# Kernel tuning notes

Hardware: AMD Instinct MI355X
Metric: run time of the kernel (lower is better)

The kernel has to match this reference:

```python
import jax, jax.numpy as jnp
import numpy as np

N_NODES = 20000
N_EDGES = 320000
NUM_FEATURES = 128
HIDDEN = 128
NUM_CLASSES = 40
GRID_SIZE = 4
SPLINE_ORDER = 3
NB = GRID_SIZE + SPLINE_ORDER  # basis functions per input feature
_H = 2.0 / GRID_SIZE  # grid_range [-1, 1]
GRID = jnp.arange(-SPLINE_ORDER, GRID_SIZE + SPLINE_ORDER + 1, dtype=jnp.float32) * _H - 1.0


def b_splines(x):
    # x: (N, in) -> (N, in, NB) via Cox-de Boor recursion (efficient-KAN)
    xg = x[..., None]
    b = ((xg >= GRID[:-1]) & (xg < GRID[1:])).astype(x.dtype)
    for k in range(1, SPLINE_ORDER + 1):
        b = ((xg - GRID[: -(k + 1)]) / (GRID[k:-1] - GRID[: -(k + 1)]) * b[..., :-1]
             + (GRID[k + 1:] - xg) / (GRID[k + 1:] - GRID[1:-k]) * b[..., 1:])
    return b


def kan_linear(x, base_w, spline_w):
    # base branch: silu(x) @ W_base^T ; spline branch: contraction over (in, NB)
    base = jax.nn.silu(x) @ base_w.T
    spline = jnp.einsum('nik,oik->no', b_splines(x), spline_w)
    return base + spline


def gcn_conv(h, base_w, spline_w, bias, src_f, dst_f, norm):
    h = kan_linear(h, base_w, spline_w)
    msg = h[src_f] * norm[:, None]  # gather + edge scaling
    out = jax.ops.segment_sum(msg, dst_f, num_segments=N_NODES)
    return out + bias


def batchnorm(h, gamma, beta):
    mean = h.mean(axis=0)
    var = h.var(axis=0)  # biased, as torch BN uses for normalization
    return (h - mean) * jax.lax.rsqrt(var + 1e-5) * gamma + beta


def setup_inputs() -> dict:
    key = jax.random.key(0)
    ks = jax.random.split(key, 8)
    s = 0.1
    return {
        'x': jax.random.normal(ks[0], (N_NODES, NUM_FEATURES), dtype=jnp.float32),
        'edge_index': jax.random.randint(ks[1], (2, N_EDGES), 0, N_NODES, dtype=jnp.int64),
        'base_w0': jax.random.normal(ks[2], (HIDDEN, NUM_FEATURES), dtype=jnp.float32) * s,
        'spline_w0': jax.random.normal(ks[3], (HIDDEN, NUM_FEATURES, NB), dtype=jnp.float32) * s,
        'bias0': jnp.zeros((HIDDEN,), dtype=jnp.float32),
        'base_w1': jax.random.normal(ks[4], (HIDDEN, HIDDEN), dtype=jnp.float32) * s,
        'spline_w1': jax.random.normal(ks[5], (HIDDEN, HIDDEN, NB), dtype=jnp.float32) * s,
        'bias1': jnp.zeros((HIDDEN,), dtype=jnp.float32),
        'base_w_out': jax.random.normal(ks[6], (NUM_CLASSES, NUM_FEATURES + 2 * HIDDEN), dtype=jnp.float32) * s,
        'spline_w_out': jax.random.normal(ks[7], (NUM_CLASSES, NUM_FEATURES + 2 * HIDDEN, NB), dtype=jnp.float32) * s,
        'bias_out': jnp.zeros((NUM_CLASSES,), dtype=jnp.float32),
        'gamma': jnp.ones((HIDDEN,), dtype=jnp.float32),
        'beta': jnp.zeros((HIDDEN,), dtype=jnp.float32),
    }


def reference(x, edge_index, base_w0, spline_w0, bias0, base_w1, spline_w1, bias1,
              base_w_out, spline_w_out, bias_out, gamma, beta):
    # gcn_norm with self loops (computed once, reused by every layer)
    loop = jnp.arange(N_NODES, dtype=edge_index.dtype)
    src_f = jnp.concatenate([edge_index[0], loop])
    dst_f = jnp.concatenate([edge_index[1], loop])
    deg = jax.ops.segment_sum(jnp.ones_like(dst_f, dtype=x.dtype), dst_f, num_segments=N_NODES)
    dinv = jnp.where(deg > 0, jax.lax.rsqrt(jnp.maximum(deg, 1e-12)), 0.0)
    norm = dinv[src_f] * dinv[dst_f]

    skips = [x]
    h = x
    for bw, sw, b in ((base_w0, spline_w0, bias0), (base_w1, spline_w1, bias1)):
        h = gcn_conv(h, bw, sw, b, src_f, dst_f, norm)
        h = batchnorm(h, gamma, beta)  # shared BN, dropout p=0.0 is identity
        skips.append(h)
    h = jnp.concatenate(skips, axis=1)  # (N, 128 + 2*128)
    return gcn_conv(h, base_w_out, spline_w_out, bias_out, src_f, dst_f, norm)
```

## Files before the change

kernel.cpp:

```cpp
#include <hip/hip_runtime.h>

#define NN 20000

typedef _Float16 half8 __attribute__((ext_vector_type(8)));
typedef _Float16 half2v __attribute__((ext_vector_type(2)));
typedef float floatx16 __attribute__((ext_vector_type(16)));

#define MFMA32(a, b, c) __builtin_amdgcn_mfma_f32_32x32x16_f16((a), (b), (c), 0, 0, 0)
#define LD8(p) (*(const half8*)(p))

__device__ __forceinline__ void bspline7_fast(float x, float b[7]) {
  float u = (x + 2.5f) * 2.0f;
  float cf = floorf(u);
  int c = (int)cf;
  float t = u - cf;
  float omt = 1.0f - t;
  float t2 = t * t, t3 = t2 * t;
  float w0 = omt * omt * omt * (1.0f / 6.0f);
  float w1 = (3.0f * t3 - 6.0f * t2 + 4.0f) * (1.0f / 6.0f);
  float w2 = (-3.0f * t3 + 3.0f * t2 + 3.0f * t + 1.0f) * (1.0f / 6.0f);
  float w3 = t3 * (1.0f / 6.0f);
  bool valid = (c >= 0) && (c <= 9);
#pragma unroll
  for (int i = 0; i < 7; ++i) {
    int d = c - i;
    float w = (d == 0) ? w3 : (d == 1) ? w2 : (d == 2) ? w1 : (d == 3) ? w0 : 0.0f;
    b[i] = valid ? w : 0.0f;
  }
}

__device__ __forceinline__ float silu_f(float x) {
  return x * (1.0f / (1.0f + __expf(-x)));
}

__device__ __forceinline__ half8 afrag(float xv) {
  float b[7];
  bspline7_fast(xv, b);
  half8 hv;
  hv[0] = (_Float16)silu_f(xv);
#pragma unroll
  for (int k = 0; k < 7; ++k) hv[k + 1] = (_Float16)b[k];
  return hv;
}

__global__ void packw_all(const float* __restrict__ Wb0, const float* __restrict__ Ws0,
                          const float* __restrict__ Wb1, const float* __restrict__ Ws1,
                          const float* __restrict__ WbO, const float* __restrict__ WsO,
                          _Float16* __restrict__ WPA0, _Float16* __restrict__ WPA1,
                          _Float16* __restrict__ WPC, int* __restrict__ degE,
                          float* __restrict__ ssb) {
  int bid = blockIdx.x;
  if (bid < 1536) {
    int s = (bid >= 768) ? 1 : 0;
    int idx = (bid - s * 768) * 256 + threadIdx.x;
    if (idx >= 196608) return;
    const float* Wb = s ? Wb1 : Wb0;
    const float* Wsp = s ? Ws1 : Ws0;
    _Float16* WP = s ? WPA1 : WPA0;
    int j = idx & 7;
    int lane = (idx >> 3) & 63;
    int u = idx >> 9;
    int cb = u % 6, ks = u / 6;
    int i = ks * 2 + (lane >> 5);
    int o32 = lane & 31;
    float v = 0.0f;
    if (cb < 4) {
      int o = cb * 32 + o32;
      v = (j == 0) ? Wb[(size_t)o * 128 + i] : Wsp[(size_t)o * 896 + i * 7 + (j - 1)];
    } else {
      int o = (cb - 4) * 32 + o32;
      if (o < 40)
        v = (j == 0) ? WbO[(size_t)o * 384 + s * 128 + i]
                     : WsO[(size_t)o * 2688 + s * 896 + i * 7 + (j - 1)];
    }
    WP[idx] = (_Float16)v;
  } else if (bid < 1792) {
    int idx = (bid - 1536) * 256 + threadIdx.x;
    if (idx >= 65536) return;
    int j = idx & 7;
    int lane = (idx >> 3) & 63;
    int u = idx >> 9;
    int cb = u & 1, ks = u >> 1;
    int i = ks * 2 + (lane >> 5);
    int o = cb * 32 + (lane & 31);
    float v = 0.0f;
    if (o < 40)
      v = (j == 0) ? WbO[(size_t)o * 384 + 2 * 128 + i]
                   : WsO[(size_t)o * 2688 + 2 * 896 + i * 7 + (j - 1)];
    WPC[idx] = (_Float16)v;
  } else if (bid < 1871) {
    int idx = (bid - 1792) * 256 + threadIdx.x;
    if (idx < NN) degE[idx] = 0;
  } else {
    int t = threadIdx.x;
    ssb[t] = (t < 128) ? 1.0f : 0.0f;
  }
}

__global__ void count_deg(const int* __restrict__ dst, int* __restrict__ degE, int E) {
  int e = blockIdx.x * 256 + threadIdx.x;
  if (e < E) atomicAdd(&degE[dst[e]], 1);
}

__global__ void build_meta2(const int* __restrict__ degE, int* __restrict__ rowptr,
                            int* __restrict__ cursor, float* __restrict__ dinv, int n) {
  __shared__ int wsum[16];
  int tid = threadIdx.x, lane = tid & 63, wid = tid >> 6;
  int i0 = tid * 20;
  int d[20];
  int s = 0;
#pragma unroll
  for (int j = 0; j < 20; ++j) {
    int i = i0 + j;
    int v = (i < n) ? degE[i] : 0;
    d[j] = v;
    s += v;
    if (i < n) dinv[i] = rsqrtf((float)(v + 1));
  }
  int val = s;
#pragma unroll
  for (int off = 1; off < 64; off <<= 1) {
    int t = __shfl_up(val, off);
    if (lane >= off) val += t;
  }
  if (lane == 63) wsum[wid] = val;
  __syncthreads();
  if (wid == 0) {
    int wv = (lane < 16) ? wsum[lane] : 0;
#pragma unroll
    for (int off = 1; off < 16; off <<= 1) {
      int t = __shfl_up(wv, off);
      if (lane >= off) wv += t;
    }
    if (lane < 16) wsum[lane] = wv;
  }
  __syncthreads();
  int base = (wid ? wsum[wid - 1] : 0) + val - s;
  if (tid == 0) rowptr[0] = 0;
#pragma unroll
  for (int j = 0; j < 20; ++j) {
    int i = i0 + j;
    if (i < n) {
      cursor[i] = base;
      rowptr[i + 1] = base + d[j];
      base += d[j];
    }
  }
}

__global__ void fill_csr(const int* __restrict__ src, const int* __restrict__ dst,
                         int* __restrict__ cursor, int* __restrict__ csr, int E) {
  int e = blockIdx.x * 256 + threadIdx.x;
  if (e < E) {
    int p = atomicAdd(&cursor[dst[e]], 1);
    csr[p] = src[e];
  }
}

__global__ __launch_bounds__(768) void gemmSA(const float* __restrict__ X,
                                              const float* __restrict__ ss,
                                              const _Float16* __restrict__ WP,
                                              const float* __restrict__ dinv,
                                              _Float16* __restrict__ A, float* __restrict__ P) {
  __shared__ _Float16 Fs[32 * 1024];
  int tid = threadIdx.x;
  int lane = tid & 63, w = tid >> 6;
  int cb = w % 6, kh = w / 6;
  int row0 = blockIdx.x * 32;
  for (int idx = tid; idx < 4096; idx += 768) {
    int r = idx >> 7, i = idx & 127;
    float xv = X[(size_t)(row0 + r) * 128 + i] * ss[i] + ss[128 + i];
    *(half8*)(Fs + ((size_t)r * 128 + (i ^ (r & 7))) * 8) = afrag(xv);
  }
  __syncthreads();

  int r = lane & 31, hi = lane >> 5, rx = r & 7;
  const _Float16* Fr = Fs + (size_t)r * 1024;
  const _Float16* Bp = WP + ((size_t)cb * 64 + lane) * 8;
  floatx16 acc = {};
  int ks0 = kh * 32;
#pragma unroll 4
  for (int ks = ks0; ks < ks0 + 32; ++ks) {
    half8 a = LD8(Fr + (size_t)((2 * ks + hi) ^ rx) * 8);
    half8 b = LD8(Bp + (size_t)ks * 3072);
    acc = MFMA32(a, b, acc);
  }
  __syncthreads();
  float* red = (float*)Fs;
  if (kh == 1) {
#pragma unroll
    for (int q = 0; q < 16; ++q) red[q * 384 + cb * 64 + lane] = acc[q];
  }
  __syncthreads();
  if (kh == 0) {
    int col = lane & 31;
#pragma unroll
    for (int q = 0; q < 16; ++q) {
      float v = acc[q] + red[q * 384 + cb * 64 + lane];
      int rl = (q & 3) + 8 * (q >> 2) + 4 * hi;
      if (cb < 4)
        A[(size_t)(row0 + rl) * 128 + cb * 32 + col] = (_Float16)(v * dinv[row0 + rl]);
      else
        P[(size_t)(row0 + rl) * 64 + (cb - 4) * 32 + col] = v;
    }
  }
}

__global__ __launch_bounds__(512) void gemmSC(const float* __restrict__ X,
                                              const float* __restrict__ ss,
                                              const _Float16* __restrict__ WP,
                                              const float* __restrict__ P0,
                                              const float* __restrict__ P1,
                                              const float* __restrict__ dinv,
                                              _Float16* __restrict__ C) {
  __shared__ _Float16 Fs[32 * 1024];
  int tid = threadIdx.x;
  int lane = tid & 63, w = tid >> 6;
  int cb = w & 1, kh = w >> 1;
  int row0 = blockIdx.x * 32;
  for (int idx = tid; idx < 4096; idx += 512) {
    int r = idx >> 7, i = idx & 127;
    float xv = X[(size_t)(row0 + r) * 128 + i] * ss[i] + ss[128 + i];
    *(half8*)(Fs + ((size_t)r * 128 + (i ^ (r & 7))) * 8) = afrag(xv);
  }
  __syncthreads();

  int r = lane & 31, hi = lane >> 5, rx = r & 7;
  const _Float16* Fr = Fs + (size_t)r * 1024;
  const _Float16* Bp = WP + ((size_t)cb * 64 + lane) * 8;
  floatx16 acc = {};
  int ks0 = kh * 16;
#pragma unroll 4
  for (int ks = ks0; ks < ks0 + 16; ++ks) {
    half8 a = LD8(Fr + (size_t)((2 * ks + hi) ^ rx) * 8);
    half8 b = LD8(Bp + (size_t)ks * 1024);
    acc = MFMA32(a, b, acc);
  }
  __syncthreads();
  float* red = (float*)Fs;
  if (kh > 0) {
#pragma unroll
    for (int q = 0; q < 16; ++q)
      red[((kh - 1) * 16 + q) * 128 + cb * 64 + lane] = acc[q];
  }
  __syncthreads();
  if (kh == 0) {
    int col = lane & 31;
#pragma unroll
    for (int q = 0; q < 16; ++q) {
      float v = acc[q] + red[q * 128 + cb * 64 + lane] +
                red[(16 + q) * 128 + cb * 64 + lane] + red[(32 + q) * 128 + cb * 64 + lane];
      int rl = (q & 3) + 8 * (q >> 2) + 4 * hi;
      size_t idx = (size_t)(row0 + rl) * 64 + cb * 32 + col;
      C[idx] = (_Float16)((v + P0[idx] + P1[idx]) * dinv[row0 + rl]);
    }
  }
}

__global__ __launch_bounds__(256) void aggregate128h(const _Float16* __restrict__ Ah,
                                                     const int* __restrict__ rowptr,
                                                     const int* __restrict__ csr,
                                                     const float* __restrict__ dinv,
                                                     const float* __restrict__ bias,
                                                     float* __restrict__ Y) {
  int wid = threadIdx.x >> 6, lane = threadIdx.x & 63;
  int n = blockIdx.x * 4 + wid;
  float di = dinv[n];
  half2v self = *(const half2v*)(Ah + (size_t)n * 128 + lane * 2);
  float a0 = (float)self[0], a1 = (float)self[1];
  float b0x = 0, b0y = 0, b1x = 0, b1y = 0, b2x = 0, b2y = 0, b3x = 0, b3y = 0;
  int e0 = rowptr[n], m = rowptr[n + 1] - e0;
  int j = 0;
  for (; j + 4 <= m; j += 4) {
    int s0 = csr[e0 + j], s1 = csr[e0 + j + 1], s2 = csr[e0 + j + 2], s3 = csr[e0 + j + 3];
    half2v r0 = *(const half2v*)(Ah + (size_t)s0 * 128 + lane * 2);
    half2v r1 = *(const half2v*)(Ah + (size_t)s1 * 128 + lane * 2);
    half2v r2 = *(const half2v*)(Ah + (size_t)s2 * 128 + lane * 2);
    half2v r3 = *(const half2v*)(Ah + (size_t)s3 * 128 + lane * 2);
    b0x += (float)r0[0]; b0y += (float)r0[1];
    b1x += (float)r1[0]; b1y += (float)r1[1];
    b2x += (float)r2[0]; b2y += (float)r2[1];
    b3x += (float)r3[0]; b3y += (float)r3[1];
  }
  for (; j < m; ++j) {
    int s = csr[e0 + j];
    half2v rr = *(const half2v*)(Ah + (size_t)s * 128 + lane * 2);
    b0x += (float)rr[0]; b0y += (float)rr[1];
  }
  a0 += (b0x + b1x) + (b2x + b3x);
  a1 += (b0y + b1y) + (b2y + b3y);
  float2 outv = {a0 * di + bias[lane * 2], a1 * di + bias[lane * 2 + 1]};
  *(float2*)(Y + (size_t)n * 128 + lane * 2) = outv;
}

__global__ __launch_bounds__(256) void aggregate40h(const _Float16* __restrict__ Ch,
                                                    const int* __restrict__ rowptr,
                                                    const int* __restrict__ csr,
                                                    const float* __restrict__ dinv,
                                                    const float* __restrict__ bias,
                                                    float* __restrict__ out) {
  int wid = threadIdx.x >> 6, lane = threadIdx.x & 63;
  int n = blockIdx.x * 4 + wid;
  float di = dinv[n];
  float a = (float)Ch[(size_t)n * 64 + lane];
  float b0 = 0, b1 = 0, b2 = 0, b3 = 0;
  int e0 = rowptr[n], m = rowptr[n + 1] - e0;
  int j = 0;
  for (; j + 4 <= m; j += 4) {
    int s0 = csr[e0 + j], s1 = csr[e0 + j + 1], s2 = csr[e0 + j + 2], s3 = csr[e0 + j + 3];
    b0 += (float)Ch[(size_t)s0 * 64 + lane];
    b1 += (float)Ch[(size_t)s1 * 64 + lane];
    b2 += (float)Ch[(size_t)s2 * 64 + lane];
    b3 += (float)Ch[(size_t)s3 * 64 + lane];
  }
  for (; j < m; ++j) {
    int s = csr[e0 + j];
    b0 += (float)Ch[(size_t)s * 64 + lane];
  }
  a += (b0 + b1) + (b2 + b3);
  if (lane < 40) out[(size_t)n * 40 + lane] = a * di + bias[lane];
}

__global__ __launch_bounds__(256) void bn_stats(const float* __restrict__ H,
                                                float* __restrict__ partial) {
  int tid = threadIdx.x;
  int c4 = (tid & 31) * 4;
  int r0 = blockIdx.x * 32 + (tid >> 5) * 4;
  float s0 = 0, s1 = 0, s2 = 0, s3 = 0, q0 = 0, q1 = 0, q2 = 0, q3 = 0;
#pragma unroll
  for (int j = 0; j < 4; ++j) {
    float4 v = *(const float4*)(H + (size_t)(r0 + j) * 128 + c4);
    s0 += v.x; s1 += v.y; s2 += v.z; s3 += v.w;
    q0 += v.x * v.x; q1 += v.y * v.y; q2 += v.z * v.z; q3 += v.w * v.w;
  }
  __shared__ float sh[2][256][4];
  sh[0][tid][0] = s0; sh[0][tid][1] = s1; sh[0][tid][2] = s2; sh[0][tid][3] = s3;
  sh[1][tid][0] = q0; sh[1][tid][1] = q1; sh[1][tid][2] = q2; sh[1][tid][3] = q3;
  __syncthreads();
  if (tid < 32) {
    float a0 = 0, a1 = 0, a2 = 0, a3 = 0, b0 = 0, b1 = 0, b2 = 0, b3 = 0;
#pragma unroll
    for (int g = 0; g < 8; ++g) {
      int u = g * 32 + tid;
      a0 += sh[0][u][0]; a1 += sh[0][u][1]; a2 += sh[0][u][2]; a3 += sh[0][u][3];
      b0 += sh[1][u][0]; b1 += sh[1][u][1]; b2 += sh[1][u][2]; b3 += sh[1][u][3];
    }
    float* p = partial + (size_t)blockIdx.x * 256;
    p[tid * 4 + 0] = a0; p[tid * 4 + 1] = a1; p[tid * 4 + 2] = a2; p[tid * 4 + 3] = a3;
    p[128 + tid * 4 + 0] = b0; p[128 + tid * 4 + 1] = b1;
    p[128 + tid * 4 + 2] = b2; p[128 + tid * 4 + 3] = b3;
  }
}

__global__ __launch_bounds__(256) void bn_reduce(const float* __restrict__ partial,
                                                 float* __restrict__ p2) {
  int tid = threadIdx.x;
  const float* base = partial + (size_t)blockIdx.x * 25 * 256 + tid;
  float a0 = 0, a1 = 0, a2 = 0, a3 = 0, a4 = 0;
#pragma unroll
  for (int j = 0; j < 5; ++j) {
    a0 += base[(j * 5 + 0) * 256];
    a1 += base[(j * 5 + 1) * 256];
    a2 += base[(j * 5 + 2) * 256];
    a3 += base[(j * 5 + 3) * 256];
    a4 += base[(j * 5 + 4) * 256];
  }
  p2[(size_t)blockIdx.x * 256 + tid] = ((a0 + a1) + (a2 + a3)) + a4;
}

__global__ __launch_bounds__(256) void bn_final2(const float* __restrict__ p2,
                                                 const float* __restrict__ gamma,
                                                 const float* __restrict__ beta,
                                                 float* __restrict__ ss) {
  int tid = threadIdx.x;
  double a0 = 0, a1 = 0, a2 = 0, a3 = 0, a4 = 0;
#pragma unroll
  for (int j = 0; j < 5; ++j) {
    a0 += (double)p2[(size_t)(j * 5 + 0) * 256 + tid];
    a1 += (double)p2[(size_t)(j * 5 + 1) * 256 + tid];
    a2 += (double)p2[(size_t)(j * 5 + 2) * 256 + tid];
    a3 += (double)p2[(size_t)(j * 5 + 3) * 256 + tid];
    a4 += (double)p2[(size_t)(j * 5 + 4) * 256 + tid];
  }
  double tot = ((a0 + a1) + (a2 + a3)) + a4;
  __shared__ double sh[256];
  sh[tid] = tot;
  __syncthreads();
  if (tid < 128) {
    double S = sh[tid];
    double Q = sh[128 + tid];
    double mean = S / (double)NN;
    double var = Q / (double)NN - mean * mean;
    float sc = gamma[tid] * rsqrtf((float)var + 1e-5f);
    ss[tid] = sc;
    ss[128 + tid] = beta[tid] - (float)mean * sc;
  }
}

extern "C" void kernel_launch(void* const* d_in, const int* in_sizes, int n_in,
                              void* d_out, int out_size, void* d_ws, size_t ws_size,
                              hipStream_t stream) {
  const float* x = (const float*)d_in[0];
  const int* ei = (const int*)d_in[1];
  const float* bw0 = (const float*)d_in[2];
  const float* sw0 = (const float*)d_in[3];
  const float* b0 = (const float*)d_in[4];
  const float* bw1 = (const float*)d_in[5];
  const float* sw1 = (const float*)d_in[6];
  const float* b1 = (const float*)d_in[7];
  const float* bwo = (const float*)d_in[8];
  const float* swo = (const float*)d_in[9];
  const float* bo = (const float*)d_in[10];
  const float* gamma = (const float*)d_in[11];
  const float* beta = (const float*)d_in[12];
  const int E = in_sizes[1] / 2;
  const int* esrc = ei;
  const int* edst = ei + E;

  char* ws = (char*)d_ws;
  size_t off = 0;
  auto alloc = [&](size_t bytes) -> void* {
    void* p = ws + off;
    off = (off + bytes + 255) & ~(size_t)255;
    return p;
  };
  _Float16* WPA0 = (_Float16*)alloc(196608 * 2);
  _Float16* WPA1 = (_Float16*)alloc(196608 * 2);
  _Float16* WPC = (_Float16*)alloc(65536 * 2);
  float* dinv = (float*)alloc(NN * 4);
  int* degE = (int*)alloc(NN * 4);
  int* rowptr = (int*)alloc((NN + 1) * 4);
  int* cursor = (int*)alloc(NN * 4);
  int* csr = (int*)alloc((size_t)E * 4);
  _Float16* A = (_Float16*)alloc((size_t)NN * 128 * 2);
  float* h1 = (float*)alloc((size_t)NN * 128 * 4);
  float* P0 = (float*)alloc((size_t)NN * 64 * 4);
  float* P1 = (float*)alloc((size_t)NN * 64 * 4);
  _Float16* Ch = (_Float16*)alloc((size_t)NN * 64 * 2);
  float* partial = (float*)alloc((size_t)625 * 256 * 4);
  float* p2 = (float*)alloc((size_t)25 * 256 * 4);
  float* ssb = (float*)alloc(256 * 4);
  float* h2 = h1;
  (void)ws_size; (void)n_in; (void)out_size;

  int egrid = (E + 255) / 256;
  const int GG = 625;

  packw_all<<<1872, 256, 0, stream>>>(bw0, sw0, bw1, sw1, bwo, swo, WPA0, WPA1, WPC,
                                      degE, ssb);
  count_deg<<<egrid, 256, 0, stream>>>(edst, degE, E);
  build_meta2<<<1, 1024, 0, stream>>>(degE, rowptr, cursor, dinv, NN);
  fill_csr<<<egrid, 256, 0, stream>>>(esrc, edst, cursor, csr, E);

  gemmSA<<<GG, 768, 0, stream>>>(x, ssb, WPA0, dinv, A, P0);
  aggregate128h<<<5000, 256, 0, stream>>>(A, rowptr, csr, dinv, b0, h1);
  bn_stats<<<625, 256, 0, stream>>>(h1, partial);
  bn_reduce<<<25, 256, 0, stream>>>(partial, p2);
  bn_final2<<<1, 256, 0, stream>>>(p2, gamma, beta, ssb);

  gemmSA<<<GG, 768, 0, stream>>>(h1, ssb, WPA1, dinv, A, P1);
  aggregate128h<<<5000, 256, 0, stream>>>(A, rowptr, csr, dinv, b1, h2);
  bn_stats<<<625, 256, 0, stream>>>(h2, partial);
  bn_reduce<<<25, 256, 0, stream>>>(partial, p2);
  bn_final2<<<1, 256, 0, stream>>>(p2, gamma, beta, ssb);

  gemmSC<<<GG, 512, 0, stream>>>(h2, ssb, WPC, P0, P1, dinv, Ch);
  aggregate40h<<<5000, 256, 0, stream>>>(Ch, rowptr, csr, dinv, bo, (float*)d_out);
}
```

Baseline: 240.3 us.

## Precompute spline feature tiles in separate kernel and stream into LDS via global_load_lds

Moves the B-spline/SiLU feature expansion out of the GEMM kernels into a standalone elementwise kernel that writes an fp16 feature tensor (N x 1024) to global memory. The GEMM kernels then copy their tile straight into shared memory with global_load_lds, so the GEMM waves no longer spend ALU time on basis evaluation. The cost is three extra kernel launches and a round trip through global memory of about 40 MB per layer (written once, read once).

```diff
diff --git a/kernel.cpp b/kernel.cpp
--- a/kernel.cpp
+++ b/kernel.cpp
@@ -8,6 +8,11 @@
 
 #define MFMA32(a, b, c) __builtin_amdgcn_mfma_f32_32x32x16_f16((a), (b), (c), 0, 0, 0)
 #define LD8(p) (*(const half8*)(p))
+
+__device__ __forceinline__ void gl_lds16(const _Float16* g, _Float16* l) {
+  __builtin_amdgcn_global_load_lds((const __attribute__((address_space(1))) char*)g,
+                                   (__attribute__((address_space(3))) char*)l, 16, 0, 0);
+}
 
 __device__ __forceinline__ void bspline7_fast(float x, float b[7]) {
   float u = (x + 2.5f) * 2.0f;
@@ -41,6 +46,15 @@
 #pragma unroll
   for (int k = 0; k < 7; ++k) hv[k + 1] = (_Float16)b[k];
   return hv;
+}
+
+__global__ void fb_kernel(const float* __restrict__ X, const float* __restrict__ ss,
+                          _Float16* __restrict__ F) {
+  int idx = blockIdx.x * 256 + threadIdx.x;
+  if (idx >= NN * 128) return;
+  int n = idx >> 7, i = idx & 127;
+  float xv = X[idx] * ss[i] + ss[128 + i];
+  *(half8*)(F + ((size_t)n * 128 + (i ^ (n & 7))) * 8) = afrag(xv);
 }
 
 __global__ void packw_all(const float* __restrict__ Wb0, const float* __restrict__ Ws0,
@@ -157,8 +171,7 @@
   }
 }
 
-__global__ __launch_bounds__(768) void gemmSA(const float* __restrict__ X,
-                                              const float* __restrict__ ss,
+__global__ __launch_bounds__(768) void gemmTG(const _Float16* __restrict__ Fg,
                                               const _Float16* __restrict__ WP,
                                               const float* __restrict__ dinv,
                                               _Float16* __restrict__ A, float* __restrict__ P) {
@@ -167,22 +180,19 @@
   int lane = tid & 63, w = tid >> 6;
   int cb = w % 6, kh = w / 6;
   int row0 = blockIdx.x * 32;
-  for (int idx = tid; idx < 4096; idx += 768) {
-    int r = idx >> 7, i = idx & 127;
-    float xv = X[(size_t)(row0 + r) * 128 + i] * ss[i] + ss[128 + i];
-    *(half8*)(Fs + ((size_t)r * 128 + (i ^ (r & 7))) * 8) = afrag(xv);
-  }
+  const _Float16* Ft = Fg + (size_t)row0 * 1024;
+  for (int i = w; i < 64; i += 12) gl_lds16(Ft + (size_t)i * 512 + lane * 8, Fs + (size_t)i * 512);
   __syncthreads();
 
   int r = lane & 31, hi = lane >> 5, rx = r & 7;
   const _Float16* Fr = Fs + (size_t)r * 1024;
-  const _Float16* Bp = WP + ((size_t)cb * 64 + lane) * 8;
+  int ks0 = kh * 32;
+  const _Float16* Bp = WP + (size_t)ks0 * 3072 + ((size_t)cb * 64 + lane) * 8;
   floatx16 acc = {};
-  int ks0 = kh * 32;
 #pragma unroll 4
-  for (int ks = ks0; ks < ks0 + 32; ++ks) {
-    half8 a = LD8(Fr + (size_t)((2 * ks + hi) ^ rx) * 8);
-    half8 b = LD8(Bp + (size_t)ks * 3072);
+  for (int k = 0; k < 32; ++k) {
+    half8 a = LD8(Fr + (size_t)((2 * (ks0 + k) + hi) ^ rx) * 8);
+    half8 b = LD8(Bp + (size_t)k * 3072);
     acc = MFMA32(a, b, acc);
   }
   __syncthreads();
@@ -206,34 +216,30 @@
   }
 }
 
-__global__ __launch_bounds__(512) void gemmSC(const float* __restrict__ X,
-                                              const float* __restrict__ ss,
-                                              const _Float16* __restrict__ WP,
-                                              const float* __restrict__ P0,
-                                              const float* __restrict__ P1,
-                                              const float* __restrict__ dinv,
-                                              _Float16* __restrict__ C) {
+__global__ __launch_bounds__(512) void gemmTC2(const _Float16* __restrict__ Fg,
+                                               const _Float16* __restrict__ WP,
+                                               const float* __restrict__ P0,
+                                               const float* __restrict__ P1,
+                                               const float* __restrict__ dinv,
+                                               _Float16* __restrict__ C) {
   __shared__ _Float16 Fs[32 * 1024];
   int tid = threadIdx.x;
   int lane = tid & 63, w = tid >> 6;
   int cb = w & 1, kh = w >> 1;
   int row0 = blockIdx.x * 32;
-  for (int idx = tid; idx < 4096; idx += 512) {
-    int r = idx >> 7, i = idx & 127;
-    float xv = X[(size_t)(row0 + r) * 128 + i] * ss[i] + ss[128 + i];
-    *(half8*)(Fs + ((size_t)r * 128 + (i ^ (r & 7))) * 8) = afrag(xv);
-  }
+  const _Float16* Ft = Fg + (size_t)row0 * 1024;
+  for (int i = w; i < 64; i += 8) gl_lds16(Ft + (size_t)i * 512 + lane * 8, Fs + (size_t)i * 512);
   __syncthreads();
 
   int r = lane & 31, hi = lane >> 5, rx = r & 7;
   const _Float16* Fr = Fs + (size_t)r * 1024;
-  const _Float16* Bp = WP + ((size_t)cb * 64 + lane) * 8;
+  int ks0 = kh * 16;
+  const _Float16* Bp = WP + (size_t)ks0 * 1024 + ((size_t)cb * 64 + lane) * 8;
   floatx16 acc = {};
-  int ks0 = kh * 16;
 #pragma unroll 4
-  for (int ks = ks0; ks < ks0 + 16; ++ks) {
-    half8 a = LD8(Fr + (size_t)((2 * ks + hi) ^ rx) * 8);
-    half8 b = LD8(Bp + (size_t)ks * 1024);
+  for (int k = 0; k < 16; ++k) {
+    half8 a = LD8(Fr + (size_t)((2 * (ks0 + k) + hi) ^ rx) * 8);
+    half8 b = LD8(Bp + (size_t)k * 1024);
     acc = MFMA32(a, b, acc);
   }
   __syncthreads();
@@ -432,6 +438,7 @@
   int* rowptr = (int*)alloc((NN + 1) * 4);
   int* cursor = (int*)alloc(NN * 4);
   int* csr = (int*)alloc((size_t)E * 4);
+  _Float16* Fg = (_Float16*)alloc((size_t)NN * 1024 * 2);
   _Float16* A = (_Float16*)alloc((size_t)NN * 128 * 2);
   float* h1 = (float*)alloc((size_t)NN * 128 * 4);
   float* P0 = (float*)alloc((size_t)NN * 64 * 4);
@@ -452,18 +459,21 @@
   build_meta2<<<1, 1024, 0, stream>>>(degE, rowptr, cursor, dinv, NN);
   fill_csr<<<egrid, 256, 0, stream>>>(esrc, edst, cursor, csr, E);
 
-  gemmSA<<<GG, 768, 0, stream>>>(x, ssb, WPA0, dinv, A, P0);
+  fb_kernel<<<10000, 256, 0, stream>>>(x, ssb, Fg);
+  gemmTG<<<GG, 768, 0, stream>>>(Fg, WPA0, dinv, A, P0);
   aggregate128h<<<5000, 256, 0, stream>>>(A, rowptr, csr, dinv, b0, h1);
   bn_stats<<<625, 256, 0, stream>>>(h1, partial);
   bn_reduce<<<25, 256, 0, stream>>>(partial, p2);
   bn_final2<<<1, 256, 0, stream>>>(p2, gamma, beta, ssb);
 
-  gemmSA<<<GG, 768, 0, stream>>>(h1, ssb, WPA1, dinv, A, P1);
+  fb_kernel<<<10000, 256, 0, stream>>>(h1, ssb, Fg);
+  gemmTG<<<GG, 768, 0, stream>>>(Fg, WPA1, dinv, A, P1);
   aggregate128h<<<5000, 256, 0, stream>>>(A, rowptr, csr, dinv, b1, h2);
   bn_stats<<<625, 256, 0, stream>>>(h2, partial);
   bn_reduce<<<25, 256, 0, stream>>>(partial, p2);
   bn_final2<<<1, 256, 0, stream>>>(p2, gamma, beta, ssb);
 
-  gemmSC<<<GG, 512, 0, stream>>>(h2, ssb, WPC, P0, P1, dinv, Ch);
+  fb_kernel<<<10000, 256, 0, stream>>>(h2, ssb, Fg);
+  gemmTC2<<<GG, 512, 0, stream>>>(Fg, WPC, P0, P1, dinv, Ch);
   aggregate40h<<<5000, 256, 0, stream>>>(Ch, rowptr, csr, dinv, bo, (float*)d_out);
 }
```

After: 253.1 us. 1.05x slower.
